# Kernel optimization log

Hardware: AMD Instinct MI355X
Metric: run time of the kernel (lower is better)

The kernel has to match this reference:

```python
import jax, jax.numpy as jnp
import numpy as np

N_NODES = 1_000_000
N_EDGES = 8_000_000


def _gcn_conv(x, src, dst, norm, W, b, n):
    # PyG GCNConv: x' = D^-1/2 (A + I) D^-1/2 (x W) + b
    h = x @ W                          # [N, out]
    msg = h[src] * norm[:, None]       # gather + edge-wise scale, [E', out]
    agg = jax.ops.segment_sum(msg, dst, num_segments=n)
    return agg + b


def setup_inputs() -> dict:
    key = jax.random.key(0)
    ks = jax.random.split(key, 6)
    F, H, O = 3, 32, 2
    x = jax.random.normal(ks[0], (N_NODES, F), dtype=jnp.float32)
    edge_index = jax.random.randint(ks[1], (2, N_EDGES), 0, N_NODES, dtype=jnp.int32)
    W1 = jax.random.normal(ks[2], (F, H), dtype=jnp.float32) * 0.3
    b1 = jnp.zeros((H,), jnp.float32)
    W2 = jax.random.normal(ks[3], (H, H), dtype=jnp.float32) * 0.15
    b2 = jnp.zeros((H,), jnp.float32)
    W3 = jax.random.normal(ks[4], (H, O), dtype=jnp.float32) * 0.15
    b3 = jnp.zeros((O,), jnp.float32)
    return {"x": x, "edge_index": edge_index, "W1": W1, "b1": b1,
            "W2": W2, "b2": b2, "W3": W3, "b3": b3}


def reference(x, edge_index, W1, b1, W2, b2, W3, b3):
    n = x.shape[0]
    loop = jnp.arange(n, dtype=edge_index.dtype)
    src = jnp.concatenate([edge_index[0], loop])  # add self-loops
    dst = jnp.concatenate([edge_index[1], loop])
    # symmetric degree normalization on A + I
    deg = jax.ops.segment_sum(jnp.ones_like(dst, dtype=x.dtype), dst, num_segments=n)
    dinv = jnp.where(deg > 0, jax.lax.rsqrt(deg), 0.0)
    norm = dinv[src] * dinv[dst]                  # [E + N]

    h = jax.nn.relu(_gcn_conv(x, src, dst, norm, W1, b1, n))
    h = jax.nn.relu(_gcn_conv(h, src, dst, norm, W2, b2, n))
    return h @ W3 + b3
```

## Files before the change

### kernel.cpp

```cpp
#include <hip/hip_runtime.h>


typedef unsigned int u32;
typedef unsigned char u8;

static __device__ __forceinline__ u32 bf16rn(float f) {
    u32 u = __float_as_uint(f);
    u += 0x7FFFu + ((u >> 16) & 1u);
    return u >> 16;
}
static __device__ __forceinline__ u32 pack_bf16(float a, float b) {
    return bf16rn(a) | (bf16rn(b) << 16);
}
static __device__ __forceinline__ float bflo(u32 w) { return __uint_as_float(w << 16); }
static __device__ __forceinline__ float bfhi(u32 w) { return __uint_as_float(w & 0xFFFF0000u); }

__global__ void zero_u32_kernel(u32* __restrict__ p, int n) {
    int i = blockIdx.x * blockDim.x + threadIdx.x;
    if (i < n) p[i] = 0u;
}

__global__ void deg_pos_kernel(const int* __restrict__ dst, u32* __restrict__ cnt,
                               u8* __restrict__ pos8, int E) {
    int e = blockIdx.x * blockDim.x + threadIdx.x;
    if (e >= E) return;
    u32 old = atomicAdd(&cnt[dst[e]], 1u);
    pos8[e] = (u8)old;
}

__global__ void scan_k1(const u32* __restrict__ cnt, u32* __restrict__ rowptr,
                        u32* __restrict__ bsum, int N) {
    __shared__ u32 sdata[256];
    int tid = threadIdx.x;
    int base = blockIdx.x * 4096 + tid * 16;
    u32 v[16], pre[16], s = 0;
#pragma unroll
    for (int k = 0; k < 16; ++k) {
        int idx = base + k;
        v[k] = (idx < N) ? cnt[idx] : 0u;
        pre[k] = s; s += v[k];
    }
    sdata[tid] = s; __syncthreads();
    for (int off = 1; off < 256; off <<= 1) {
        u32 t = (tid >= off) ? sdata[tid - off] : 0u;
        __syncthreads();
        sdata[tid] += t;
        __syncthreads();
    }
    u32 excl = sdata[tid] - s;
#pragma unroll
    for (int k = 0; k < 16; ++k) {
        int idx = base + k;
        if (idx < N) rowptr[idx] = excl + pre[k];
    }
    if (tid == 255) bsum[blockIdx.x] = sdata[255];
}

__global__ void scan_k2(const u32* __restrict__ bsum, u32* __restrict__ boff, int NB) {
    __shared__ u32 sdata[256];
    int tid = threadIdx.x;
    u32 s = (tid < NB) ? bsum[tid] : 0u;
    sdata[tid] = s; __syncthreads();
    for (int off = 1; off < 256; off <<= 1) {
        u32 t = (tid >= off) ? sdata[tid - off] : 0u;
        __syncthreads();
        sdata[tid] += t;
        __syncthreads();
    }
    if (tid < NB) boff[tid] = sdata[tid] - s;
}

__global__ void finalize_kernel(u32* __restrict__ rowptr, const u32* __restrict__ boff,
                                const u32* __restrict__ cnt, const float* __restrict__ x,
                                float* __restrict__ dinv, float4* __restrict__ u4, int N) {
    int i = blockIdx.x * blockDim.x + threadIdx.x;
    if (i >= N) return;
    u32 r = rowptr[i] + boff[i >> 12];
    rowptr[i] = r;
    if (i == N - 1) rowptr[N] = r + cnt[i];
    float iv = rsqrtf((float)cnt[i] + 1.0f);
    dinv[i] = iv;
    u4[i] = make_float4(x[i * 3 + 0] * iv, x[i * 3 + 1] * iv, x[i * 3 + 2] * iv, 0.0f);
}

__global__ void scatter_kernel(const int* __restrict__ src, const int* __restrict__ dst,
                               const u8* __restrict__ pos8, const u32* __restrict__ rowptr,
                               int* __restrict__ srec, int E) {
    int e = blockIdx.x * blockDim.x + threadIdx.x;
    if (e >= E) return;
    u32 slot = rowptr[dst[e]] + (u32)pos8[e];
    srec[slot] = src[e];
}

__global__ void l1_kernel(const u32* __restrict__ rowptr, const int* __restrict__ srec,
                          const float4* __restrict__ u4, const float* __restrict__ dinv,
                          const float* __restrict__ W1, const float* __restrict__ b1,
                          u32* __restrict__ g1u, int N) {
    __shared__ float sW1[96];
    __shared__ float sb1[32];
    if (threadIdx.x < 96) sW1[threadIdx.x] = W1[threadIdx.x];
    if (threadIdx.x < 32) sb1[threadIdx.x] = b1[threadIdx.x];
    __syncthreads();
    int i = blockIdx.x * blockDim.x + threadIdx.x;
    if (i >= N) return;
    float iv = dinv[i];
    float4 u = u4[i];
    float a0 = u.x, a1 = u.y, a2 = u.z;
    u32 beg = rowptr[i], end = rowptr[i + 1];
    for (u32 t = beg; t < end; ++t) {
        float4 us = u4[srec[t]];
        a0 += us.x; a1 += us.y; a2 += us.z;
    }
    a0 *= iv; a1 *= iv; a2 *= iv;
    u32 packed[16];
#pragma unroll
    for (int jj = 0; jj < 16; ++jj) {
        int j0 = 2 * jj, j1 = 2 * jj + 1;
        float v0 = fmaf(a0, sW1[j0], fmaf(a1, sW1[32 + j0], fmaf(a2, sW1[64 + j0], sb1[j0])));
        float v1 = fmaf(a0, sW1[j1], fmaf(a1, sW1[32 + j1], fmaf(a2, sW1[64 + j1], sb1[j1])));
        v0 = fmaxf(v0, 0.0f) * iv;
        v1 = fmaxf(v1, 0.0f) * iv;
        packed[jj] = pack_bf16(v0, v1);
    }
    uint4* dp = (uint4*)(g1u + (size_t)i * 16);
    const uint4* pp = (const uint4*)packed;
    dp[0] = pp[0]; dp[1] = pp[1]; dp[2] = pp[2]; dp[3] = pp[3];
}

__global__ void l2_fused_kernel(const u32* __restrict__ rowptr, const int* __restrict__ srec,
                                const u32* __restrict__ g1u, const float* __restrict__ dinv,
                                const float* __restrict__ W2, const float* __restrict__ b2,
                                const float* __restrict__ W3, const float* __restrict__ b3,
                                float* __restrict__ out, int N) {
    const int lane = threadIdx.x & 63;
    const int l32  = lane & 31;
    const int h    = lane >> 5;
    const int fl   = l32 & 7;
    const int esub = l32 >> 3;

    float w2col[32];
#pragma unroll
    for (int k = 0; k < 32; ++k) w2col[k] = W2[k * 32 + l32];
    const float b2j = b2[l32];
    const float w30 = W3[2 * l32 + 0];
    const float w31 = W3[2 * l32 + 1];
    const float b30 = b3[0], b31 = b3[1];

    const int nWaves = (gridDim.x * blockDim.x) >> 6;
    const int waveId = (blockIdx.x * blockDim.x + threadIdx.x) >> 6;

    for (int base = waveId * 2; base < N; base += nWaves * 2) {
        const int node = base + h;
        const bool valid = node < N;
        u32 beg = 0; int deg = 0;
        if (valid) {
            uint2 rp = *(const uint2*)(rowptr + node);
            beg = rp.x; deg = (int)(rp.y - rp.x);
        }
        float a0 = 0.0f, a1 = 0.0f, a2 = 0.0f, a3 = 0.0f;
        if (valid && esub == 0) {
            uint2 w = *(const uint2*)(g1u + (size_t)node * 16 + 2 * fl);
            a0 = bflo(w.x); a1 = bfhi(w.x); a2 = bflo(w.y); a3 = bfhi(w.y);
        }
        int mdeg = max(deg, __shfl_xor(deg, 32));
        for (int q0 = 0; q0 < mdeg; q0 += 32) {
            int navail = deg - q0;
            navail = navail < 0 ? 0 : (navail > 32 ? 32 : navail);
            int sv = (l32 < navail) ? srec[beg + q0 + l32] : 0;
            int mnav = max(navail, __shfl_xor(navail, 32));
            for (int q = 0; q < mnav; q += 4) {
                int eidx = q + esub;
                int s = __shfl(sv, eidx, 32);
                if (eidx < navail) {
                    uint2 w = *(const uint2*)(g1u + (size_t)s * 16 + 2 * fl);
                    a0 += bflo(w.x); a1 += bfhi(w.x);
                    a2 += bflo(w.y); a3 += bfhi(w.y);
                }
            }
        }
        a0 += __shfl_xor(a0, 8);  a1 += __shfl_xor(a1, 8);
        a2 += __shfl_xor(a2, 8);  a3 += __shfl_xor(a3, 8);
        a0 += __shfl_xor(a0, 16); a1 += __shfl_xor(a1, 16);
        a2 += __shfl_xor(a2, 16); a3 += __shfl_xor(a3, 16);
        float iv = valid ? dinv[node] : 0.0f;
        a0 *= iv; a1 *= iv; a2 *= iv; a3 *= iv;

        float hh = b2j;
#pragma unroll
        for (int f = 0; f < 8; ++f) {
            hh = fmaf(__shfl(a0, f, 32), w2col[4 * f + 0], hh);
            hh = fmaf(__shfl(a1, f, 32), w2col[4 * f + 1], hh);
            hh = fmaf(__shfl(a2, f, 32), w2col[4 * f + 2], hh);
            hh = fmaf(__shfl(a3, f, 32), w2col[4 * f + 3], hh);
        }
        hh = fmaxf(hh, 0.0f);
        float p0 = hh * w30, p1 = hh * w31;
        p0 += __shfl_xor(p0, 1);  p1 += __shfl_xor(p1, 1);
        p0 += __shfl_xor(p0, 2);  p1 += __shfl_xor(p1, 2);
        p0 += __shfl_xor(p0, 4);  p1 += __shfl_xor(p1, 4);
        p0 += __shfl_xor(p0, 8);  p1 += __shfl_xor(p1, 8);
        p0 += __shfl_xor(p0, 16); p1 += __shfl_xor(p1, 16);
        if (valid && l32 == 0)
            *(float2*)(out + (size_t)node * 2) = make_float2(p0 + b30, p1 + b31);
    }
}

extern "C" void kernel_launch(void* const* d_in, const int* in_sizes, int n_in,
                              void* d_out, int out_size, void* d_ws, size_t ws_size,
                              hipStream_t stream) {
    const float* x  = (const float*)d_in[0];
    const int*   ei = (const int*)d_in[1];
    const float* W1 = (const float*)d_in[2];
    const float* b1 = (const float*)d_in[3];
    const float* W2 = (const float*)d_in[4];
    const float* b2 = (const float*)d_in[5];
    const float* W3 = (const float*)d_in[6];
    const float* b3 = (const float*)d_in[7];
    float* out = (float*)d_out;

    const int N = in_sizes[0] / 3;
    const int E = in_sizes[1] / 2;
    const int* src = ei;
    const int* dst = ei + E;

    auto align256 = [](size_t v) { return (v + 255) & ~(size_t)255; };
    char* ws = (char*)d_ws;
    size_t off = 0;
    int*    srec   = (int*)   (ws + off); off = align256(off + (size_t)E * 4);
    u32*    g1u    = (u32*)   (ws + off); off = align256(off + (size_t)N * 16 * 4);
    float4* u4     = (float4*)(ws + off); off = align256(off + (size_t)N * 16);
    u8*     pos8   = (u8*)    (ws + off); off = align256(off + (size_t)E);
    u32*    rowptr = (u32*)   (ws + off); off = align256(off + (size_t)(N + 1) * 4);
    u32*    cnt    = (u32*)   (ws + off); off = align256(off + (size_t)N * 4);
    float*  dinv   = (float*) (ws + off); off = align256(off + (size_t)N * 4);
    u32*    bsum   = (u32*)   (ws + off); off = align256(off + 256 * 4);
    u32*    boff   = (u32*)   (ws + off); off = align256(off + 256 * 4);
    (void)ws_size;

    const int B = 256;
    const int NB = (N + 4095) / 4096;

    zero_u32_kernel<<<(N + B - 1) / B, B, 0, stream>>>(cnt, N);
    deg_pos_kernel<<<(E + B - 1) / B, B, 0, stream>>>(dst, cnt, pos8, E);
    scan_k1<<<NB, B, 0, stream>>>(cnt, rowptr, bsum, N);
    scan_k2<<<1, B, 0, stream>>>(bsum, boff, NB);
    finalize_kernel<<<(N + B - 1) / B, B, 0, stream>>>(rowptr, boff, cnt, x, dinv, u4, N);
    scatter_kernel<<<(E + B - 1) / B, B, 0, stream>>>(src, dst, pos8, rowptr, srec, E);
    l1_kernel<<<(N + B - 1) / B, B, 0, stream>>>(rowptr, srec, u4, dinv, W1, b1, g1u, N);
    l2_fused_kernel<<<2048, B, 0, stream>>>(rowptr, srec, g1u, dinv, W2, b2, W3, b3, out, N);
}
```

Baseline: 1.205 ms.

## Prefetch next node's CSR data in layer-2 loop, recompute dinv, unroll layer-1 gather

```diff
diff --git a/kernel.cpp b/kernel.cpp
--- a/kernel.cpp
+++ b/kernel.cpp
@@ -72,14 +72,13 @@
 
 __global__ void finalize_kernel(u32* __restrict__ rowptr, const u32* __restrict__ boff,
                                 const u32* __restrict__ cnt, const float* __restrict__ x,
-                                float* __restrict__ dinv, float4* __restrict__ u4, int N) {
+                                float4* __restrict__ u4, int N) {
     int i = blockIdx.x * blockDim.x + threadIdx.x;
     if (i >= N) return;
     u32 r = rowptr[i] + boff[i >> 12];
     rowptr[i] = r;
     if (i == N - 1) rowptr[N] = r + cnt[i];
     float iv = rsqrtf((float)cnt[i] + 1.0f);
-    dinv[i] = iv;
     u4[i] = make_float4(x[i * 3 + 0] * iv, x[i * 3 + 1] * iv, x[i * 3 + 2] * iv, 0.0f);
 }
 
@@ -93,7 +92,7 @@
 }
 
 __global__ void l1_kernel(const u32* __restrict__ rowptr, const int* __restrict__ srec,
-                          const float4* __restrict__ u4, const float* __restrict__ dinv,
+                          const float4* __restrict__ u4,
                           const float* __restrict__ W1, const float* __restrict__ b1,
                           u32* __restrict__ g1u, int N) {
     __shared__ float sW1[96];
@@ -103,13 +102,21 @@
     __syncthreads();
     int i = blockIdx.x * blockDim.x + threadIdx.x;
     if (i >= N) return;
-    float iv = dinv[i];
+    u32 beg = rowptr[i], end = rowptr[i + 1];
+    float iv = rsqrtf((float)(end - beg) + 1.0f);
     float4 u = u4[i];
     float a0 = u.x, a1 = u.y, a2 = u.z;
-    u32 beg = rowptr[i], end = rowptr[i + 1];
-    for (u32 t = beg; t < end; ++t) {
-        float4 us = u4[srec[t]];
-        a0 += us.x; a1 += us.y; a2 += us.z;
+    u32 t = beg;
+    for (; t + 4 <= end; t += 4) {
+        int s0 = srec[t], s1 = srec[t + 1], s2 = srec[t + 2], s3 = srec[t + 3];
+        float4 f0 = u4[s0], f1 = u4[s1], f2 = u4[s2], f3 = u4[s3];
+        a0 += (f0.x + f1.x) + (f2.x + f3.x);
+        a1 += (f0.y + f1.y) + (f2.y + f3.y);
+        a2 += (f0.z + f1.z) + (f2.z + f3.z);
+    }
+    for (; t < end; ++t) {
+        float4 f = u4[srec[t]];
+        a0 += f.x; a1 += f.y; a2 += f.z;
     }
     a0 *= iv; a1 *= iv; a2 *= iv;
     u32 packed[16];
@@ -128,7 +135,7 @@
 }
 
 __global__ void l2_fused_kernel(const u32* __restrict__ rowptr, const int* __restrict__ srec,
-                                const u32* __restrict__ g1u, const float* __restrict__ dinv,
+                                const u32* __restrict__ g1u,
                                 const float* __restrict__ W2, const float* __restrict__ b2,
                                 const float* __restrict__ W3, const float* __restrict__ b3,
                                 float* __restrict__ out, int N) {
@@ -146,31 +153,46 @@
     const float w31 = W3[2 * l32 + 1];
     const float b30 = b3[0], b31 = b3[1];
 
-    const int nWaves = (gridDim.x * blockDim.x) >> 6;
-    const int waveId = (blockIdx.x * blockDim.x + threadIdx.x) >> 6;
-
-    for (int base = waveId * 2; base < N; base += nWaves * 2) {
-        const int node = base + h;
-        const bool valid = node < N;
-        u32 beg = 0; int deg = 0;
-        if (valid) {
-            uint2 rp = *(const uint2*)(rowptr + node);
-            beg = rp.x; deg = (int)(rp.y - rp.x);
+    const int nWaves  = (gridDim.x * blockDim.x) >> 6;
+    const int stride2 = nWaves * 2;
+    int base = ((blockIdx.x * blockDim.x + threadIdx.x) >> 6) * 2;
+
+    int  node  = base + h;
+    bool valid = node < N;
+    uint2 rp = valid ? *(const uint2*)(rowptr + node) : make_uint2(0u, 0u);
+    int  deg  = (int)(rp.y - rp.x);
+    int  sv   = (valid && l32 < (deg < 32 ? deg : 32)) ? srec[rp.x + l32] : 0;
+    uint2 selfw = make_uint2(0u, 0u);
+    if (valid && esub == 0) selfw = *(const uint2*)(g1u + (size_t)node * 16 + 2 * fl);
+
+    for (; base < N; base += stride2) {
+        const int   cnode  = base + h;
+        const bool  cvalid = cnode < N;
+        const uint2 crp    = rp;
+        const int   cdeg   = deg;
+        const int   csv    = sv;
+        const uint2 cself  = selfw;
+
+        const int  nbase  = base + stride2;
+        const int  nnode  = nbase + h;
+        const bool nvalid = nnode < N;
+        rp = nvalid ? *(const uint2*)(rowptr + nnode) : make_uint2(0u, 0u);
+
+        float a0 = 0.0f, a1 = 0.0f, a2 = 0.0f, a3 = 0.0f;
+        if (esub == 0) {
+            a0 = bflo(cself.x); a1 = bfhi(cself.x);
+            a2 = bflo(cself.y); a3 = bfhi(cself.y);
         }
-        float a0 = 0.0f, a1 = 0.0f, a2 = 0.0f, a3 = 0.0f;
-        if (valid && esub == 0) {
-            uint2 w = *(const uint2*)(g1u + (size_t)node * 16 + 2 * fl);
-            a0 = bflo(w.x); a1 = bfhi(w.x); a2 = bflo(w.y); a3 = bfhi(w.y);
-        }
-        int mdeg = max(deg, __shfl_xor(deg, 32));
+        int mdeg = max(cdeg, __shfl_xor(cdeg, 32));
         for (int q0 = 0; q0 < mdeg; q0 += 32) {
-            int navail = deg - q0;
+            int navail = cdeg - q0;
             navail = navail < 0 ? 0 : (navail > 32 ? 32 : navail);
-            int sv = (l32 < navail) ? srec[beg + q0 + l32] : 0;
+            int svq = (q0 == 0) ? csv
+                                : ((l32 < navail) ? srec[crp.x + q0 + l32] : 0);
             int mnav = max(navail, __shfl_xor(navail, 32));
             for (int q = 0; q < mnav; q += 4) {
                 int eidx = q + esub;
-                int s = __shfl(sv, eidx, 32);
+                int s = __shfl(svq, eidx, 32);
                 if (eidx < navail) {
                     uint2 w = *(const uint2*)(g1u + (size_t)s * 16 + 2 * fl);
                     a0 += bflo(w.x); a1 += bfhi(w.x);
@@ -178,11 +200,17 @@
                 }
             }
         }
+
+        deg = (int)(rp.y - rp.x);
+        sv  = (nvalid && l32 < (deg < 32 ? deg : 32)) ? srec[rp.x + l32] : 0;
+        selfw = make_uint2(0u, 0u);
+        if (nvalid && esub == 0) selfw = *(const uint2*)(g1u + (size_t)nnode * 16 + 2 * fl);
+
         a0 += __shfl_xor(a0, 8);  a1 += __shfl_xor(a1, 8);
         a2 += __shfl_xor(a2, 8);  a3 += __shfl_xor(a3, 8);
         a0 += __shfl_xor(a0, 16); a1 += __shfl_xor(a1, 16);
         a2 += __shfl_xor(a2, 16); a3 += __shfl_xor(a3, 16);
-        float iv = valid ? dinv[node] : 0.0f;
+        float iv = rsqrtf((float)cdeg + 1.0f);
         a0 *= iv; a1 *= iv; a2 *= iv; a3 *= iv;
 
         float hh = b2j;
@@ -200,8 +228,8 @@
         p0 += __shfl_xor(p0, 4);  p1 += __shfl_xor(p1, 4);
         p0 += __shfl_xor(p0, 8);  p1 += __shfl_xor(p1, 8);
         p0 += __shfl_xor(p0, 16); p1 += __shfl_xor(p1, 16);
-        if (valid && l32 == 0)
-            *(float2*)(out + (size_t)node * 2) = make_float2(p0 + b30, p1 + b31);
+        if (cvalid && l32 == 0)
+            *(float2*)(out + (size_t)cnode * 2) = make_float2(p0 + b30, p1 + b31);
     }
 }
 
@@ -232,7 +260,6 @@
     u8*     pos8   = (u8*)    (ws + off); off = align256(off + (size_t)E);
     u32*    rowptr = (u32*)   (ws + off); off = align256(off + (size_t)(N + 1) * 4);
     u32*    cnt    = (u32*)   (ws + off); off = align256(off + (size_t)N * 4);
-    float*  dinv   = (float*) (ws + off); off = align256(off + (size_t)N * 4);
     u32*    bsum   = (u32*)   (ws + off); off = align256(off + 256 * 4);
     u32*    boff   = (u32*)   (ws + off); off = align256(off + 256 * 4);
     (void)ws_size;
@@ -244,8 +271,8 @@
     deg_pos_kernel<<<(E + B - 1) / B, B, 0, stream>>>(dst, cnt, pos8, E);
     scan_k1<<<NB, B, 0, stream>>>(cnt, rowptr, bsum, N);
     scan_k2<<<1, B, 0, stream>>>(bsum, boff, NB);
-    finalize_kernel<<<(N + B - 1) / B, B, 0, stream>>>(rowptr, boff, cnt, x, dinv, u4, N);
+    finalize_kernel<<<(N + B - 1) / B, B, 0, stream>>>(rowptr, boff, cnt, x, u4, N);
     scatter_kernel<<<(E + B - 1) / B, B, 0, stream>>>(src, dst, pos8, rowptr, srec, E);
-    l1_kernel<<<(N + B - 1) / B, B, 0, stream>>>(rowptr, srec, u4, dinv, W1, b1, g1u, N);
-    l2_fused_kernel<<<2048, B, 0, stream>>>(rowptr, srec, g1u, dinv, W2, b2, W3, b3, out, N);
-}
+    l1_kernel<<<(N + B - 1) / B, B, 0, stream>>>(rowptr, srec, u4, W1, b1, g1u, N);
+    l2_fused_kernel<<<2048, B, 0, stream>>>(rowptr, srec, g1u, W2, b2, W3, b3, out, N);
+}
```

Measured after the change: 1.166 ms. -3.3%, faster.
